# Performance work log

Measured on AMD Instinct MI355X. Metric: run time of the kernel, lower is better.

## Reference

```python
import jax, jax.numpy as jnp
import numpy as np

N_TOKEN = 64
H = 16
D = 1024
D_K = 64
D_V = 64
S3 = 30  # 3 * S, number of gated leading positions
GATE_INIT = 10.0


def setup_inputs() -> dict:
    key = jax.random.key(0)
    ks = jax.random.split(key, 8)
    B, L = 32, 2048
    x = jax.random.normal(ks[0], (B, L, D), dtype=jnp.float32)
    q_init = (1.0 / D_K) ** 0.5
    q_tok = jax.random.uniform(ks[1], (1, N_TOKEN, D), minval=-q_init, maxval=q_init, dtype=jnp.float32)
    scale = 0.02
    Wq = jax.random.normal(ks[2], (D, H * D_K), dtype=jnp.float32) * scale
    Wk = jax.random.normal(ks[3], (D, H * D_K), dtype=jnp.float32) * scale
    Wv = jax.random.normal(ks[4], (D, H * D_V), dtype=jnp.float32) * scale
    Wfc = jax.random.normal(ks[5], (H * D_V, D), dtype=jnp.float32) * scale
    gate_logit = -jnp.ones((S3,), dtype=jnp.float32) * GATE_INIT  # matches module init
    gamma = jnp.ones((D,), dtype=jnp.float32)
    beta = jnp.zeros((D,), dtype=jnp.float32)
    return {"x": x, "q_tok": q_tok, "Wq": Wq, "Wk": Wk, "Wv": Wv, "Wfc": Wfc,
            "gate_logit": gate_logit, "gamma": gamma, "beta": beta}


def reference(x, q_tok, Wq, Wk, Wv, Wfc, gate_logit, gamma, beta):
    # x: [B, L, D]; q_tok: [1, n_token, D]. Dropout is identity (eval mode).
    B, L, _ = x.shape
    temp = D_K ** 0.5

    # Cumulative-product gate over the first 30 positions (the torch for-loop).
    gate = jnp.cumprod(1.0 - jax.nn.sigmoid(gate_logit))  # [30]
    x1 = x.at[:, :S3].multiply(gate[None, :, None])

    q = (q_tok @ Wq).reshape(N_TOKEN, H, D_K)          # [n, H, dk]
    k = (x @ Wk).reshape(B, L, H, D_K)                  # [B, L, H, dk]
    v = (x1 @ Wv).reshape(B, L, H, D_V)                 # [B, L, H, dv]

    scores = jnp.einsum('nhd,blhd->bhnl', q / temp, k)  # [B, H, n, L]
    attn = jax.nn.softmax(scores, axis=-1)
    out = jnp.einsum('bhnl,blhd->bnhd', attn, v).reshape(B, N_TOKEN, H * D_V)

    out = out @ Wfc + q_tok                              # residual with query tokens

    # LayerNorm over last dim, eps=1e-6
    mu = jnp.mean(out, axis=-1, keepdims=True)
    var = jnp.mean(jnp.square(out - mu), axis=-1, keepdims=True)
    out = (out - mu) * jax.lax.rsqrt(var + 1e-6) * gamma + beta
    return out
```

## Files before the change

### kernel.cpp

```cpp
#include <hip/hip_runtime.h>
#include <stdint.h>

typedef unsigned short u16;
typedef short bf16x8 __attribute__((ext_vector_type(8)));
typedef float f32x4 __attribute__((ext_vector_type(4)));

__device__ __forceinline__ u16 f2b(float f) {
  uint32_t u = __builtin_bit_cast(uint32_t, f);
  u += 0x7fffu + ((u >> 16) & 1u);
  return (u16)(u >> 16);
}

__device__ __forceinline__ void gload_lds16(const void* g, void* l) {
  __builtin_amdgcn_global_load_lds(
      (const __attribute__((address_space(1))) void*)g,
      (__attribute__((address_space(3))) void*)l, 16, 0, 0);
}

__global__ void gate_kernel(const float* __restrict__ gl, float* __restrict__ gate) {
  if (threadIdx.x == 0 && blockIdx.x == 0) {
    float g = 1.0f;
    for (int i = 0; i < 30; ++i) {
      float s = 1.0f / (1.0f + __expf(-gl[i]));
      g *= (1.0f - s);
      gate[i] = g;
    }
  }
}

__global__ __launch_bounds__(256) void cvt_kernel(const float* __restrict__ src,
                                                  u16* __restrict__ dst) {
  int64_t i = ((int64_t)blockIdx.x * 256 + threadIdx.x) * 8;
  float4 a = *(const float4*)(src + i);
  float4 b = *(const float4*)(src + i + 4);
  union { u16 u[8]; bf16x8 v; } o;
  o.u[0] = f2b(a.x); o.u[1] = f2b(a.y); o.u[2] = f2b(a.z); o.u[3] = f2b(a.w);
  o.u[4] = f2b(b.x); o.u[5] = f2b(b.y); o.u[6] = f2b(b.z); o.u[7] = f2b(b.w);
  *(bf16x8*)(dst + i) = o.v;
}

__global__ __launch_bounds__(256) void transpose_w_kernel(const float* __restrict__ src,
                                                          u16* __restrict__ dst) {
  __shared__ float ls[64][65];
  int t = threadIdx.x;
  int bx = blockIdx.x & 15;
  int by = blockIdx.x >> 4;
  int r0 = by * 64, c0 = bx * 64;
  int tr = t >> 6, tc = t & 63;
#pragma unroll
  for (int i = 0; i < 16; ++i)
    ls[tr + i * 4][tc] = src[(int64_t)(r0 + tr + i * 4) * 1024 + c0 + tc];
  __syncthreads();
#pragma unroll
  for (int i = 0; i < 16; ++i)
    dst[(int64_t)(c0 + tr + i * 4) * 1024 + r0 + tc] = f2b(ls[tc][tr + i * 4]);
}

__global__ __launch_bounds__(256, 4) void q_gemm_kernel(
    const u16* __restrict__ qtokb, const u16* __restrict__ wqT, u16* __restrict__ qb) {
  __shared__ u16 As[4096];
  __shared__ u16 Bs[8192];
  int n0 = blockIdx.x * 128;
  int t = threadIdx.x, w = t >> 6, lane = t & 63;
  int wn = w * 32;
  f32x4 acc[2][4] = {};
  int l3 = lane >> 3;
  int colE = ((lane & 7) ^ l3) * 8;
  const u16* aS = qtokb + (int64_t)(w * 16 + l3) * 1024 + colE;
  const u16* bS = wqT + (int64_t)(n0 + w * 32 + l3) * 1024 + colE;
  u16* aD = As + w * 1024;
  u16* bD = Bs + w * 2048;
  int l15 = lane & 15, g16 = lane >> 4;
  for (int kt = 0; kt < 16; ++kt) {
    int ko = kt * 64;
    __syncthreads();
    gload_lds16(aS + ko, aD);
    gload_lds16(aS + ko + 8192, aD + 512);
#pragma unroll
    for (int g = 0; g < 4; ++g) gload_lds16(bS + ko + g * 8192, bD + g * 512);
    __syncthreads();
#pragma unroll
    for (int kk = 0; kk < 2; ++kk) {
      int sl = ((kk * 4 + g16) ^ (l15 & 7)) * 8;
      bf16x8 af[4], bf[2];
#pragma unroll
      for (int j = 0; j < 4; ++j) af[j] = *(const bf16x8*)(As + (j * 16 + l15) * 64 + sl);
#pragma unroll
      for (int i = 0; i < 2; ++i) bf[i] = *(const bf16x8*)(Bs + (wn + i * 16 + l15) * 64 + sl);
#pragma unroll
      for (int i = 0; i < 2; ++i)
#pragma unroll
        for (int j = 0; j < 4; ++j)
          acc[i][j] = __builtin_amdgcn_mfma_f32_16x16x32_bf16(bf[i], af[j], acc[i][j], 0, 0, 0);
    }
  }
  const float sc = 1.44269504f / 8.0f;
  int lr = g16 * 4;
#pragma unroll
  for (int i = 0; i < 2; ++i) {
    int colg = n0 + wn + i * 16 + lr;
#pragma unroll
    for (int j = 0; j < 4; ++j) {
      int qrow = j * 16 + l15;
      u16 p[4];
#pragma unroll
      for (int r = 0; r < 4; ++r) p[r] = f2b(acc[i][j][r] * sc);
      *(uint64_t*)(qb + qrow * 1024 + colg) = *(uint64_t*)p;
    }
  }
}

__global__ __launch_bounds__(256) void kv_gemm_kernel(
    const u16* __restrict__ xb, const u16* __restrict__ wkvT,
    const float* __restrict__ gate, u16* __restrict__ kbuf, u16* __restrict__ vT) {
  __shared__ u16 As[4096];
  __shared__ u16 Bs[4096];
  int bid = blockIdx.x;
  int mb = bid >> 4, nb = bid & 15;
  int m0 = mb * 128, n0 = nb * 128;
  int t = threadIdx.x, w = t >> 6, lane = t & 63;
  int wm = (w >> 1) * 64, wn = (w & 1) * 64;
  bool isV = (n0 >= 1024);
  f32x4 acc[4][4] = {};
  int srow = w * 32 + (lane >> 2);
  int scol = (((lane & 3) ^ ((lane >> 2) & 3))) * 8;
  const u16* aSrc = xb + (int64_t)(m0 + srow) * 1024 + scol;
  const u16* bSrc = wkvT + (int64_t)(n0 + srow) * 1024 + scol;
  u16* aDst = As + w * 1024;
  u16* bDst = Bs + w * 1024;
  int l15 = lane & 15, g16 = lane >> 4;
  for (int kt = 0; kt < 32; ++kt) {
    __syncthreads();
    int ko = kt * 32;
    gload_lds16(aSrc + ko, aDst);
    gload_lds16(aSrc + 16 * 1024 + ko, aDst + 512);
    gload_lds16(bSrc + ko, bDst);
    gload_lds16(bSrc + 16 * 1024 + ko, bDst + 512);
    __syncthreads();
    bf16x8 af[4], bf[4];
#pragma unroll
    for (int i = 0; i < 4; ++i) {
      int row = wm + i * 16 + l15;
      af[i] = *(const bf16x8*)(As + row * 32 + ((g16 ^ (row & 3)) * 8));
    }
#pragma unroll
    for (int j = 0; j < 4; ++j) {
      int row = wn + j * 16 + l15;
      bf[j] = *(const bf16x8*)(Bs + row * 32 + ((g16 ^ (row & 3)) * 8));
    }
    if (!isV) {
#pragma unroll
      for (int i = 0; i < 4; ++i)
#pragma unroll
        for (int j = 0; j < 4; ++j)
          acc[i][j] = __builtin_amdgcn_mfma_f32_16x16x32_bf16(af[i], bf[j], acc[i][j], 0, 0, 0);
    } else {
#pragma unroll
      for (int i = 0; i < 4; ++i)
#pragma unroll
        for (int j = 0; j < 4; ++j)
          acc[i][j] = __builtin_amdgcn_mfma_f32_16x16x32_bf16(bf[i], af[j], acc[i][j], 0, 0, 0);
    }
  }
  int b = m0 >> 11, lbase = m0 & 2047;
  int lr = g16 * 4;
  if (!isV) {
#pragma unroll
    for (int i = 0; i < 4; ++i)
#pragma unroll
      for (int j = 0; j < 4; ++j) {
        int gcol = n0 + wn + j * 16 + l15;
        int h = gcol >> 6, dk = gcol & 63;
#pragma unroll
        for (int r = 0; r < 4; ++r) {
          int l = lbase + wm + i * 16 + lr + r;
          kbuf[(int64_t)((b * 16 + h) * 2048 + l) * 64 + dk] = f2b(acc[i][j][r]);
        }
      }
  } else {
#pragma unroll
    for (int j = 0; j < 4; ++j) {
      int lloc = wm + j * 16 + l15;
      int l = lbase + lloc;
      float g = 1.0f;
      if (lbase == 0 && lloc < 30) g = gate[lloc];
#pragma unroll
      for (int i = 0; i < 4; ++i) {
#pragma unroll
        for (int r = 0; r < 4; ++r) {
          int gn = (n0 - 1024) + wn + i * 16 + lr + r;
          int h = gn >> 6, dv = gn & 63;
          vT[(int64_t)((b * 16 + h) * 64 + dv) * 2048 + l] = f2b(acc[i][j][r] * g);
        }
      }
    }
  }
}

__global__ __launch_bounds__(256) void attn_kernel(
    const u16* __restrict__ qb, const u16* __restrict__ kbuf,
    const u16* __restrict__ vT, float* __restrict__ pO,
    float* __restrict__ pm, float* __restrict__ ps) {
  __shared__ u16 Ps[4096];
  int bid = blockIdx.x;
  int b = bid >> 6, h = (bid >> 2) & 15, c = bid & 3;
  int t = threadIdx.x, w = t >> 6, lane = t & 63;
  int l15 = lane & 15, g16 = lane >> 4, lh8 = g16 * 8;
  bf16x8 qf0 = *(const bf16x8*)(qb + (w * 16 + l15) * 1024 + h * 64 + lh8);
  bf16x8 qf1 = *(const bf16x8*)(qb + (w * 16 + l15) * 1024 + h * 64 + 32 + lh8);
  const u16* kB = kbuf + (int64_t)(b * 16 + h) * (2048 * 64);
  const u16* vB = vT + (int64_t)(b * 16 + h) * (64 * 2048);
  char* PsW = (char*)Ps + w * 2048;
  float m_r[4] = {-1e30f, -1e30f, -1e30f, -1e30f};
  float s_r[4] = {0.f, 0.f, 0.f, 0.f};
  f32x4 O[4] = {};
  for (int lt = 0; lt < 8; ++lt) {
    int l0 = c * 512 + lt * 64;
    f32x4 S[4];
#pragma unroll
    for (int ls = 0; ls < 4; ++ls) {
      const u16* kr = kB + (l0 + ls * 16 + l15) * 64 + lh8;
      bf16x8 k0 = *(const bf16x8*)(kr);
      bf16x8 k1 = *(const bf16x8*)(kr + 32);
      f32x4 s = {};
      s = __builtin_amdgcn_mfma_f32_16x16x32_bf16(qf0, k0, s, 0, 0, 0);
      s = __builtin_amdgcn_mfma_f32_16x16x32_bf16(qf1, k1, s, 0, 0, 0);
      S[ls] = s;
    }
    float scale[4];
#pragma unroll
    for (int r = 0; r < 4; ++r) {
      float tm = fmaxf(fmaxf(S[0][r], S[1][r]), fmaxf(S[2][r], S[3][r]));
#pragma unroll
      for (int msk = 1; msk < 16; msk <<= 1)
        tm = fmaxf(tm, __shfl_xor(tm, msk, 16));
      float mn = fmaxf(m_r[r], tm);
      scale[r] = exp2f(m_r[r] - mn);
      m_r[r] = mn;
    }
#pragma unroll
    for (int ls = 0; ls < 4; ++ls)
#pragma unroll
      for (int r = 0; r < 4; ++r) S[ls][r] = exp2f(S[ls][r] - m_r[r]);
#pragma unroll
    for (int r = 0; r < 4; ++r) {
      float psm = (S[0][r] + S[1][r]) + (S[2][r] + S[3][r]);
      s_r[r] = s_r[r] * scale[r] + psm;
    }
#pragma unroll
    for (int ls = 0; ls < 4; ++ls)
#pragma unroll
      for (int r = 0; r < 4; ++r) {
        int row = g16 * 4 + r;
        int off = (ls * 16 + l15) * 2;
        *(u16*)(PsW + row * 128 + (off ^ ((row & 7) << 4))) = f2b(S[ls][r]);
      }
#pragma unroll
    for (int d = 0; d < 4; ++d)
#pragma unroll
      for (int r = 0; r < 4; ++r) O[d][r] *= scale[r];
    bf16x8 pa0, pa1;
    {
      int off0 = g16 * 16;
      pa0 = *(const bf16x8*)(PsW + l15 * 128 + (off0 ^ ((l15 & 7) << 4)));
      pa1 = *(const bf16x8*)(PsW + l15 * 128 + ((off0 + 64) ^ ((l15 & 7) << 4)));
    }
#pragma unroll
    for (int d = 0; d < 4; ++d) {
      const u16* vr = vB + (d * 16 + l15) * 2048 + l0 + lh8;
      bf16x8 v0 = *(const bf16x8*)(vr);
      bf16x8 v1 = *(const bf16x8*)(vr + 32);
      O[d] = __builtin_amdgcn_mfma_f32_16x16x32_bf16(pa0, v0, O[d], 0, 0, 0);
      O[d] = __builtin_amdgcn_mfma_f32_16x16x32_bf16(pa1, v1, O[d], 0, 0, 0);
    }
  }
#pragma unroll
  for (int r = 0; r < 4; ++r) {
    float s = s_r[r];
#pragma unroll
    for (int msk = 1; msk < 16; msk <<= 1) s += __shfl_xor(s, msk, 16);
    s_r[r] = s;
  }
  int64_t pbase = (int64_t)bid * 4096;
#pragma unroll
  for (int d = 0; d < 4; ++d)
#pragma unroll
    for (int r = 0; r < 4; ++r) {
      int n = w * 16 + g16 * 4 + r;
      pO[pbase + n * 64 + d * 16 + l15] = O[d][r];
    }
  if (l15 == 0) {
#pragma unroll
    for (int r = 0; r < 4; ++r) {
      int n = w * 16 + g16 * 4 + r;
      pm[bid * 64 + n] = m_r[r];
      ps[bid * 64 + n] = s_r[r];
    }
  }
}

__global__ __launch_bounds__(256) void attn_combine_kernel(
    const float* __restrict__ pO, const float* __restrict__ pm,
    const float* __restrict__ ps, u16* __restrict__ attnout) {
  int bh = blockIdx.x;
  int b = bh >> 4, h = bh & 15;
  int t = threadIdx.x;
  int dv = t & 63, grp = t >> 6;
#pragma unroll
  for (int i = 0; i < 16; ++i) {
    int n = grp * 16 + i;
    int base = bh * 256 + n;
    float m0 = pm[base], m1 = pm[base + 64], m2 = pm[base + 128], m3 = pm[base + 192];
    float M = fmaxf(fmaxf(m0, m1), fmaxf(m2, m3));
    float w0 = exp2f(m0 - M), w1 = exp2f(m1 - M), w2 = exp2f(m2 - M), w3 = exp2f(m3 - M);
    float stot = w0 * ps[base] + w1 * ps[base + 64] + w2 * ps[base + 128] + w3 * ps[base + 192];
    float inv = 1.0f / stot;
    int64_t ob = (int64_t)bh * 16384 + n * 64 + dv;
    float o = w0 * pO[ob] + w1 * pO[ob + 4096] + w2 * pO[ob + 8192] + w3 * pO[ob + 12288];
    attnout[((int64_t)(b * 64 + n)) * 1024 + h * 64 + dv] = f2b(o * inv);
  }
}

__global__ __launch_bounds__(256, 4) void fc_gemm_kernel(
    const u16* __restrict__ a, const u16* __restrict__ bT,
    const float* __restrict__ q_tok, float* __restrict__ out) {
  __shared__ u16 As[8192];
  __shared__ u16 Bs[8192];
  int bid = blockIdx.x;
  int mb = bid >> 3, nb = bid & 7;
  int m0 = mb * 128, n0 = nb * 128;
  int t = threadIdx.x, w = t >> 6, lane = t & 63;
  int wm = (w >> 1) * 64, wn = (w & 1) * 64;
  f32x4 acc[4][4] = {};
  int l3 = lane >> 3;
  int colE = ((lane & 7) ^ l3) * 8;
  const u16* aS = a + (int64_t)(m0 + w * 32 + l3) * 1024 + colE;
  const u16* bS = bT + (int64_t)(n0 + w * 32 + l3) * 1024 + colE;
  u16* aD = As + w * 2048;
  u16* bD = Bs + w * 2048;
  int l15 = lane & 15, g16 = lane >> 4;
  for (int kt = 0; kt < 16; ++kt) {
    int ko = kt * 64;
    __syncthreads();
#pragma unroll
    for (int g = 0; g < 4; ++g) {
      gload_lds16(aS + ko + g * 8192, aD + g * 512);
      gload_lds16(bS + ko + g * 8192, bD + g * 512);
    }
    __syncthreads();
#pragma unroll
    for (int kk = 0; kk < 2; ++kk) {
      int sl = ((kk * 4 + g16) ^ (l15 & 7)) * 8;
      bf16x8 af[4], bf[4];
#pragma unroll
      for (int i = 0; i < 4; ++i) af[i] = *(const bf16x8*)(As + (wm + i * 16 + l15) * 64 + sl);
#pragma unroll
      for (int j = 0; j < 4; ++j) bf[j] = *(const bf16x8*)(Bs + (wn + j * 16 + l15) * 64 + sl);
#pragma unroll
      for (int i = 0; i < 4; ++i)
#pragma unroll
        for (int j = 0; j < 4; ++j)
          acc[i][j] = __builtin_amdgcn_mfma_f32_16x16x32_bf16(bf[i], af[j], acc[i][j], 0, 0, 0);
    }
  }
  int lr = g16 * 4;
#pragma unroll
  for (int i = 0; i < 4; ++i) {
    int colg = n0 + wn + i * 16 + lr;
#pragma unroll
    for (int j = 0; j < 4; ++j) {
      int row = m0 + wm + j * 16 + l15;
      float4 res = *(const float4*)(q_tok + (row & 63) * 1024 + colg);
      float4 o;
      o.x = acc[i][j][0] + res.x;
      o.y = acc[i][j][1] + res.y;
      o.z = acc[i][j][2] + res.z;
      o.w = acc[i][j][3] + res.w;
      *(float4*)(out + (int64_t)row * 1024 + colg) = o;
    }
  }
}

__global__ __launch_bounds__(256) void ln_kernel(
    const float* __restrict__ fc, const float* __restrict__ gamma,
    const float* __restrict__ beta, float* __restrict__ out) {
  __shared__ float red[8];
  int row = blockIdx.x, t = threadIdx.x;
  float4 y = *(const float4*)(fc + (int64_t)row * 1024 + t * 4);
  float s = (y.x + y.y) + (y.z + y.w);
  float ss = (y.x * y.x + y.y * y.y) + (y.z * y.z + y.w * y.w);
#pragma unroll
  for (int msk = 1; msk < 64; msk <<= 1) {
    s += __shfl_xor(s, msk, 64);
    ss += __shfl_xor(ss, msk, 64);
  }
  if ((t & 63) == 0) { red[t >> 6] = s; red[4 + (t >> 6)] = ss; }
  __syncthreads();
  s = (red[0] + red[1]) + (red[2] + red[3]);
  ss = (red[4] + red[5]) + (red[6] + red[7]);
  float mu = s * (1.0f / 1024.0f);
  float var = ss * (1.0f / 1024.0f) - mu * mu;
  float rstd = rsqrtf(var + 1e-6f);
  float4 g = *(const float4*)(gamma + t * 4);
  float4 be = *(const float4*)(beta + t * 4);
  float4 o;
  o.x = (y.x - mu) * rstd * g.x + be.x;
  o.y = (y.y - mu) * rstd * g.y + be.y;
  o.z = (y.z - mu) * rstd * g.z + be.z;
  o.w = (y.w - mu) * rstd * g.w + be.w;
  *(float4*)(out + (int64_t)row * 1024 + t * 4) = o;
}

extern "C" void kernel_launch(void* const* d_in, const int* in_sizes, int n_in,
                              void* d_out, int out_size, void* d_ws, size_t ws_size,
                              hipStream_t stream) {
  const float* x     = (const float*)d_in[0];
  const float* q_tok = (const float*)d_in[1];
  const float* Wq    = (const float*)d_in[2];
  const float* Wk    = (const float*)d_in[3];
  const float* Wv    = (const float*)d_in[4];
  const float* Wfc   = (const float*)d_in[5];
  const float* gl    = (const float*)d_in[6];
  const float* gamma = (const float*)d_in[7];
  const float* beta  = (const float*)d_in[8];
  float* out = (float*)d_out;
  char* ws = (char*)d_ws;

  u16*   xb      = (u16*)(ws);
  u16*   kbuf    = (u16*)(ws + 134217728);
  u16*   vT      = (u16*)(ws + 268435456);
  u16*   wkvT    = (u16*)(ws + 402653184);
  u16*   wfcT    = (u16*)(ws + 406847488);
  u16*   wqT     = (u16*)(ws + 408944640);
  u16*   qtokb   = (u16*)(ws + 411041792);
  u16*   qb      = (u16*)(ws + 411172864);
  float* gate    = (float*)(ws + 411303936);
  u16*   attnout = (u16*)(ws + 411304448);
  float* fcout   = (float*)(ws + 415498752);
  float* pO = (float*)(ws);
  float* pm = (float*)(ws + 33554432);
  float* ps = (float*)(ws + 34078720);

  gate_kernel<<<1, 64, 0, stream>>>(gl, gate);
  cvt_kernel<<<32768, 256, 0, stream>>>(x, xb);
  cvt_kernel<<<32, 256, 0, stream>>>(q_tok, qtokb);
  transpose_w_kernel<<<256, 256, 0, stream>>>(Wk, wkvT);
  transpose_w_kernel<<<256, 256, 0, stream>>>(Wv, wkvT + 1024 * 1024);
  transpose_w_kernel<<<256, 256, 0, stream>>>(Wfc, wfcT);
  transpose_w_kernel<<<256, 256, 0, stream>>>(Wq, wqT);
  q_gemm_kernel<<<8, 256, 0, stream>>>(qtokb, wqT, qb);
  kv_gemm_kernel<<<8192, 256, 0, stream>>>(xb, wkvT, gate, kbuf, vT);
  attn_kernel<<<2048, 256, 0, stream>>>(qb, kbuf, vT, pO, pm, ps);
  attn_combine_kernel<<<512, 256, 0, stream>>>(pO, pm, ps, attnout);
  fc_gemm_kernel<<<128, 256, 0, stream>>>(attnout, wfcT, q_tok, fcout);
  ln_kernel<<<2048, 256, 0, stream>>>(fcout, gamma, beta, out);
}
```

Baseline: 703.1 us.

## Double-buffer LDS tiles in KV GEMM to overlap global loads with MFMA

Converts the KV projection GEMM's shared-memory A/B tiles into two-stage ping-pong buffers. The next k-tile's global-to-LDS loads are issued before the current tile's MFMAs run, so there is one barrier per iteration instead of two. The intent is to hide global memory latency behind compute. In exchange it doubles LDS use per block, which can lower occupancy, and it relies on an explicit vmcnt wait for correctness.

```diff
diff --git a/kernel.cpp b/kernel.cpp
--- a/kernel.cpp
+++ b/kernel.cpp
@@ -113,8 +113,8 @@
 __global__ __launch_bounds__(256) void kv_gemm_kernel(
     const u16* __restrict__ xb, const u16* __restrict__ wkvT,
     const float* __restrict__ gate, u16* __restrict__ kbuf, u16* __restrict__ vT) {
-  __shared__ u16 As[4096];
-  __shared__ u16 Bs[4096];
+  __shared__ u16 As[2][4096];
+  __shared__ u16 Bs[2][4096];
   int bid = blockIdx.x;
   int mb = bid >> 4, nb = bid & 15;
   int m0 = mb * 128, n0 = nb * 128;
@@ -126,27 +126,39 @@
   int scol = (((lane & 3) ^ ((lane >> 2) & 3))) * 8;
   const u16* aSrc = xb + (int64_t)(m0 + srow) * 1024 + scol;
   const u16* bSrc = wkvT + (int64_t)(n0 + srow) * 1024 + scol;
-  u16* aDst = As + w * 1024;
-  u16* bDst = Bs + w * 1024;
   int l15 = lane & 15, g16 = lane >> 4;
+  {
+    u16* aD = As[0] + w * 1024;
+    u16* bD = Bs[0] + w * 1024;
+    gload_lds16(aSrc, aD);
+    gload_lds16(aSrc + 16 * 1024, aD + 512);
+    gload_lds16(bSrc, bD);
+    gload_lds16(bSrc + 16 * 1024, bD + 512);
+  }
   for (int kt = 0; kt < 32; ++kt) {
+    asm volatile("s_waitcnt vmcnt(0)" ::: "memory");
     __syncthreads();
-    int ko = kt * 32;
-    gload_lds16(aSrc + ko, aDst);
-    gload_lds16(aSrc + 16 * 1024 + ko, aDst + 512);
-    gload_lds16(bSrc + ko, bDst);
-    gload_lds16(bSrc + 16 * 1024 + ko, bDst + 512);
-    __syncthreads();
+    if (kt < 31) {
+      int ko = (kt + 1) * 32;
+      u16* aD = As[(kt + 1) & 1] + w * 1024;
+      u16* bD = Bs[(kt + 1) & 1] + w * 1024;
+      gload_lds16(aSrc + ko, aD);
+      gload_lds16(aSrc + 16 * 1024 + ko, aD + 512);
+      gload_lds16(bSrc + ko, bD);
+      gload_lds16(bSrc + 16 * 1024 + ko, bD + 512);
+    }
+    const u16* Ab = As[kt & 1];
+    const u16* Bb = Bs[kt & 1];
     bf16x8 af[4], bf[4];
 #pragma unroll
     for (int i = 0; i < 4; ++i) {
       int row = wm + i * 16 + l15;
-      af[i] = *(const bf16x8*)(As + row * 32 + ((g16 ^ (row & 3)) * 8));
+      af[i] = *(const bf16x8*)(Ab + row * 32 + ((g16 ^ (row & 3)) * 8));
     }
 #pragma unroll
     for (int j = 0; j < 4; ++j) {
       int row = wn + j * 16 + l15;
-      bf[j] = *(const bf16x8*)(Bs + row * 32 + ((g16 ^ (row & 3)) * 8));
+      bf[j] = *(const bf16x8*)(Bb + row * 32 + ((g16 ^ (row & 3)) * 8));
     }
     if (!isV) {
 #pragma unroll
```

Result: slower. 769.0 us (+9.4%).
